# Kernel optimization log

Measured on AMD Instinct MI355X. Metric: run time of the kernel, lower is better.

Reference implementation:

```python
import jax, jax.numpy as jnp
import numpy as np

B, T, C, H = 2, 2048, 1024, 16
HD = C // H  # head dim = 64


def setup_inputs() -> dict:
    key = jax.random.key(0)
    k1, k2, k3 = jax.random.split(key, 3)
    scale = 0.02
    x = jax.random.normal(k1, (B, T, C), dtype=jnp.float32)
    w_attn = jax.random.normal(k2, (C, 3 * C), dtype=jnp.float32) * scale
    b_attn = jnp.zeros((3 * C,), dtype=jnp.float32)
    w_proj = jax.random.normal(k3, (C, C), dtype=jnp.float32) * scale
    b_proj = jnp.zeros((C,), dtype=jnp.float32)
    return {"x": x, "w_attn": w_attn, "b_attn": b_attn, "w_proj": w_proj, "b_proj": b_proj}


def reference(x, w_attn, b_attn, w_proj, b_proj):
    b, t, c = x.shape
    qkv = x @ w_attn + b_attn  # [B,T,3C]
    q, k, v = jnp.split(qkv, 3, axis=-1)
    # [B,T,C] -> [B,H,T,HD]
    q = q.reshape(b, t, H, HD).transpose(0, 2, 1, 3)
    k = k.reshape(b, t, H, HD).transpose(0, 2, 1, 3)
    v = v.reshape(b, t, H, HD).transpose(0, 2, 1, 3)
    att = jnp.einsum('bhqd,bhkd->bhqk', q, k) * (1.0 / jnp.sqrt(jnp.float32(HD)))
    causal = jnp.tril(jnp.ones((t, t), dtype=bool))  # [T,T]
    att = jnp.where(causal[None, None, :, :], att, jnp.float32(-jnp.inf))
    att = jax.nn.softmax(att, axis=-1)
    y = jnp.einsum('bhqk,bhkd->bhqd', att, v)
    y = y.transpose(0, 2, 1, 3).reshape(b, t, c)
    return y @ w_proj + b_proj
```

## Files before the change

### kernel.cpp

```cpp
#include <hip/hip_runtime.h>


typedef unsigned short u16;
typedef unsigned short u16x8 __attribute__((ext_vector_type(8)));
typedef __bf16 bf16x8 __attribute__((ext_vector_type(8)));
typedef __bf16 bf16x4 __attribute__((ext_vector_type(4)));
typedef float f32x4 __attribute__((ext_vector_type(4)));

#define MFMA16(a, b, c) __builtin_amdgcn_mfma_f32_16x16x32_bf16(a, b, c, 0, 0, 0)

static __device__ __forceinline__ u16 f2b(float f) {
  union { float f; unsigned int i; } x; x.f = f;
  unsigned int r = x.i + 0x7fffu + ((x.i >> 16) & 1u);
  return (u16)(r >> 16);
}
static __device__ __forceinline__ float b2f(u16 u) {
  union { unsigned int i; float f; } x; x.i = ((unsigned int)u) << 16; return x.f;
}

static __device__ __forceinline__ void gload_lds16(const u16* g, u16* l) {
#if defined(__HIP_DEVICE_COMPILE__)
  __builtin_amdgcn_global_load_lds(
      (const __attribute__((address_space(1))) unsigned int*)g,
      (__attribute__((address_space(3))) unsigned int*)l,
      16, 0, 0);
#else
  (void)g; (void)l;
#endif
}

__global__ __launch_bounds__(256) void cast_f32_bf16(
    const float* __restrict__ in, u16* __restrict__ out) {
  int i = (blockIdx.x * 256 + threadIdx.x) * 8;
  float4 a = *(const float4*)&in[i];
  float4 b = *(const float4*)&in[i + 4];
  u16x8 o;
  o[0] = f2b(a.x); o[1] = f2b(a.y); o[2] = f2b(a.z); o[3] = f2b(a.w);
  o[4] = f2b(b.x); o[5] = f2b(b.y); o[6] = f2b(b.z); o[7] = f2b(b.w);
  *(u16x8*)&out[i] = o;
}

__global__ __launch_bounds__(256) void transpose_f32_bf16(
    const float* __restrict__ in, u16* __restrict__ out, int R, int Cc) {
  __shared__ u16 tile[32][33];
  int bx = blockIdx.x, by = blockIdx.y;
  int tx = threadIdx.x, ty = threadIdx.y;
#pragma unroll
  for (int i = 0; i < 4; i++) {
    int r = by * 32 + ty + i * 8;
    int c = bx * 32 + tx;
    tile[ty + i * 8][tx] = f2b(in[r * Cc + c]);
  }
  __syncthreads();
#pragma unroll
  for (int i = 0; i < 4; i++) {
    int r = bx * 32 + ty + i * 8;
    int c = by * 32 + tx;
    out[r * R + c] = tile[tx][ty + i * 8];
  }
}

__global__ __launch_bounds__(256) void transpose_v(
    const u16* __restrict__ in, u16* __restrict__ out) {
  int bh = blockIdx.y;
  int t = blockIdx.x * 128 + (threadIdx.x & 127);
  int dg = (threadIdx.x >> 7) * 32;
  const u16* src = in + (bh * 2048 + t) * 64;
  int p = t & 31;
  int tp = (t & ~31) | ((((p >> 2) & 3) << 3) | ((p >> 4) << 2) | (p & 3));
  u16* dst = out + bh * 64 * 2048 + tp;
#pragma unroll
  for (int i = 0; i < 32; i++) {
    int d = dg + i;
    dst[d * 2048] = src[d];
  }
}

template <int MODE>
__global__ __launch_bounds__(256, 3) void gemm_bt(
    const u16* __restrict__ A, const u16* __restrict__ Bt,
    const float* __restrict__ bias, float* __restrict__ out,
    u16* __restrict__ Qb, u16* __restrict__ Kb, u16* __restrict__ Vb,
    int M, int N, int K) {
  __shared__ u16 lA[128 * 32];
  __shared__ u16 lB[128 * 32];

  const int tid = threadIdx.x;
  const int lane = tid & 63;
  const int w = tid >> 6;
  const int wm = (w >> 1) * 64, wn = (w & 1) * 64;
  const int l15 = lane & 15, quad = lane >> 4;
  const int m0 = blockIdx.y * 128, n0 = blockIdx.x * 128;

  const int srow = lane >> 2;
  const int scol = (lane & 3) * 8;

  f32x4 acc[4][4] = {};

  for (int k0 = 0; k0 < K; k0 += 32) {
    __syncthreads();
#pragma unroll
    for (int h = 0; h < 2; h++) {
      int r = h * 64 + w * 16 + srow;
      gload_lds16(&A[(m0 + r) * K + k0 + scol], &lA[h * 2048 + w * 512 + lane * 8]);
      gload_lds16(&Bt[(n0 + r) * K + k0 + scol], &lB[h * 2048 + w * 512 + lane * 8]);
    }
    __syncthreads();

    bf16x8 af[4], bfr[4];
#pragma unroll
    for (int mi = 0; mi < 4; mi++)
      af[mi] = *(const bf16x8*)&lA[(wm + mi * 16 + l15) * 32 + quad * 8];
#pragma unroll
    for (int ni = 0; ni < 4; ni++)
      bfr[ni] = *(const bf16x8*)&lB[(wn + ni * 16 + l15) * 32 + quad * 8];
#pragma unroll
    for (int mi = 0; mi < 4; mi++)
#pragma unroll
      for (int ni = 0; ni < 4; ni++)
        acc[mi][ni] = MFMA16(af[mi], bfr[ni], acc[mi][ni]);
  }

#pragma unroll
  for (int mi = 0; mi < 4; mi++) {
#pragma unroll
    for (int ni = 0; ni < 4; ni++) {
      int n = n0 + wn + ni * 16 + l15;
      float bv = bias[n];
#pragma unroll
      for (int reg = 0; reg < 4; reg++) {
        int m = m0 + wm + mi * 16 + quad * 4 + reg;
        float v = acc[mi][ni][reg] + bv;
        if (MODE == 1) {
          out[m * N + n] = v;
        } else {
          int which = n >> 10;
          if (which == 1) v *= 0.18033688011112042f;
          int hn = n & 1023;
          int hh = hn >> 6, d = hn & 63;
          int b = m >> 11, t = m & 2047;
          u16* dst = (which == 0) ? Qb : ((which == 1) ? Kb : Vb);
          dst[(((b << 4) + hh) * 2048 + t) * 64 + d] = f2b(v);
        }
      }
    }
  }
}

__global__ __launch_bounds__(256, 4) void attn_split(
    const u16* __restrict__ Qg, const u16* __restrict__ Kg,
    const u16* __restrict__ Vt, u16* __restrict__ Yg,
    u16* __restrict__ Opart, float* __restrict__ lpart) {
  __shared__ u16 lk[2][64 * 72];
  __shared__ u16 lvt[2][64 * 72];

  const int x = blockIdx.x;
  const int bh = blockIdx.y;
  int qt, s, ns;
  if (x < 8)       { qt = x;                s = 0;            ns = 1; }
  else if (x < 24) { int r = x - 8;  qt = 8  + (r >> 1); s = r & 1; ns = 2; }
  else if (x < 48) { int r = x - 24; qt = 16 + r / 3;    s = r % 3; ns = 3; }
  else             { int r = x - 48; qt = 24 + (r >> 2); s = r & 3; ns = 4; }
  const int total = qt + 1;
  const int kts  = (s * total) / ns;
  const int kend = ((s + 1) * total) / ns;

  const int tid = threadIdx.x;
  const int lane = tid & 63;
  const int w = tid >> 6;
  const int l15 = lane & 15, quad = lane >> 4;
  const int qbase = qt * 64;
  const int base = bh * 2048 * 64;
  const int vbase = bh * 64 * 2048;
  const int qloc = w * 16 + l15;

  const int sr = tid >> 3;
  const int sc = (tid & 7) * 8;

  const u16* qrow = Qg + base + (qbase + w * 16 + l15) * 64;
  bf16x8 bq0 = *(const bf16x8*)&qrow[quad * 8];
  bf16x8 bq1 = *(const bf16x8*)&qrow[32 + quad * 8];

  u16x8 onesu = {0x3F80, 0x3F80, 0x3F80, 0x3F80, 0x3F80, 0x3F80, 0x3F80, 0x3F80};
  bf16x8 ones = *(const bf16x8*)&onesu;

  const u16* kp = Kg + base;
  const u16* vp = Vt + vbase;

  u16x8 kr[2], vr[2];
  {
    int kvb = kts * 64;
#pragma unroll
    for (int h = 0; h < 2; h++) {
      int r = sr + h * 32;
      kr[h] = *(const u16x8*)&kp[(kvb + r) * 64 + sc];
      vr[h] = *(const u16x8*)&vp[r * 2048 + kvb + sc];
    }
  }

  f32x4 oacc[4] = {};
  f32x4 lacc = {};

  int cur = 0;
  for (int kt = kts; kt < kend; kt++) {
    u16* lkc = lk[cur];
    u16* lvc = lvt[cur];
#pragma unroll
    for (int h = 0; h < 2; h++) {
      int r = sr + h * 32;
      *(u16x8*)&lkc[r * 72 + sc] = kr[h];
      *(u16x8*)&lvc[r * 72 + sc] = vr[h];
    }
    __syncthreads();
    if (kt + 1 < kend) {
      int kvb = (kt + 1) * 64;
#pragma unroll
      for (int h = 0; h < 2; h++) {
        int r = sr + h * 32;
        kr[h] = *(const u16x8*)&kp[(kvb + r) * 64 + sc];
        vr[h] = *(const u16x8*)&vp[r * 2048 + kvb + sc];
      }
    }

    const bool diag = (kt == qt);

#pragma unroll
    for (int u = 0; u < 2; u++) {
      bf16x8 pa;
#pragma unroll
      for (int half = 0; half < 2; half++) {
        int nt = 2 * u + half;
        bf16x8 ak0 = *(const bf16x8*)&lkc[(nt * 16 + l15) * 72 + quad * 8];
        bf16x8 ak1 = *(const bf16x8*)&lkc[(nt * 16 + l15) * 72 + 32 + quad * 8];
        f32x4 st = {};
        st = MFMA16(ak0, bq0, st);
        st = MFMA16(ak1, bq1, st);
#pragma unroll
        for (int reg = 0; reg < 4; reg++) {
          float sv = st[reg];
          if (diag && (nt * 16 + quad * 4 + reg) > qloc) sv = -1e30f;
          pa[half * 4 + reg] = (__bf16)__builtin_amdgcn_exp2f(sv);
        }
      }
      lacc = MFMA16(pa, ones, lacc);
#pragma unroll
      for (int dt = 0; dt < 4; dt++) {
        bf16x8 bv = *(const bf16x8*)&lvc[(dt * 16 + l15) * 72 + u * 32 + quad * 8];
        oacc[dt] = MFMA16(pa, bv, oacc[dt]);
      }
    }
    cur ^= 1;
  }

  if (ns == 1) {
    const int b = bh >> 4, hh = bh & 15;
    float inv[4];
#pragma unroll
    for (int reg = 0; reg < 4; reg++) inv[reg] = 1.0f / lacc[reg];
#pragma unroll
    for (int dt = 0; dt < 4; dt++)
#pragma unroll
      for (int reg = 0; reg < 4; reg++) {
        int q = qbase + w * 16 + quad * 4 + reg;
        int col = hh * 64 + dt * 16 + l15;
        Yg[(b * 2048 + q) * 1024 + col] = f2b(oacc[dt][reg] * inv[reg]);
      }
  } else {
    const int p = bh * 80 + x;
    u16* op = Opart + p * 4096 + (w * 16) * 64;
#pragma unroll
    for (int dt = 0; dt < 4; dt++)
#pragma unroll
      for (int reg = 0; reg < 4; reg++)
        op[(quad * 4 + reg) * 64 + dt * 16 + l15] = f2b(oacc[dt][reg]);
    if (l15 == 0) {
#pragma unroll
      for (int reg = 0; reg < 4; reg++)
        lpart[p * 64 + w * 16 + quad * 4 + reg] = lacc[reg];
    }
  }
}

__global__ __launch_bounds__(256) void attn_combine(
    const u16* __restrict__ Opart, const float* __restrict__ lpart,
    u16* __restrict__ Yg) {
  const int qt = 8 + blockIdx.x;
  const int bh = blockIdx.y;
  const int tid = threadIdx.x;
  const int row = tid >> 2;
  const int cg = (tid & 3) * 16;
  int xb, ns;
  if (qt < 16)      { xb = 8  + (qt - 8) * 2;  ns = 2; }
  else if (qt < 24) { xb = 24 + (qt - 16) * 3; ns = 3; }
  else              { xb = 48 + (qt - 24) * 4; ns = 4; }

  float acc[16] = {};
  float lsum = 0.f;
  for (int i = 0; i < ns; i++) {
    int p = bh * 80 + xb + i;
    lsum += lpart[p * 64 + row];
    const u16* oprow = Opart + p * 4096 + row * 64 + cg;
    u16x8 a = *(const u16x8*)&oprow[0];
    u16x8 b = *(const u16x8*)&oprow[8];
#pragma unroll
    for (int j = 0; j < 8; j++) { acc[j] += b2f(a[j]); acc[8 + j] += b2f(b[j]); }
  }
  float inv = 1.0f / lsum;
  u16x8 o0, o1;
#pragma unroll
  for (int j = 0; j < 8; j++) { o0[j] = f2b(acc[j] * inv); o1[j] = f2b(acc[8 + j] * inv); }
  const int b = bh >> 4, hh = bh & 15;
  u16* y = Yg + ((long)(b * 2048 + qt * 64 + row)) * 1024 + hh * 64 + cg;
  *(u16x8*)&y[0] = o0;
  *(u16x8*)&y[8] = o1;
}

__global__ __launch_bounds__(256, 4) void attn_kernel(
    const u16* __restrict__ Qg, const u16* __restrict__ Kg,
    const u16* __restrict__ Vt, u16* __restrict__ Yg) {
  __shared__ u16 lk[64 * 72];
  __shared__ u16 lvt[64 * 72];

  const int qt = 31 - blockIdx.x;
  const int bh = blockIdx.y;
  const int tid = threadIdx.x;
  const int lane = tid & 63;
  const int w = tid >> 6;
  const int l15 = lane & 15, quad = lane >> 4;
  const int qbase = qt * 64;
  const int base = bh * 2048 * 64;
  const int vbase = bh * 64 * 2048;
  const int sr = tid >> 3;
  const int sc = (tid & 7) * 8;

  const u16* qrow = Qg + base + (qbase + w * 16 + l15) * 64;
  bf16x8 bq0 = *(const bf16x8*)&qrow[quad * 8];
  bf16x8 bq1 = *(const bf16x8*)&qrow[32 + quad * 8];

  u16x8 onesu = {0x3F80, 0x3F80, 0x3F80, 0x3F80, 0x3F80, 0x3F80, 0x3F80, 0x3F80};
  bf16x8 ones = *(const bf16x8*)&onesu;

  const u16* kp = Kg + base;
  const u16* vp = Vt + vbase;

  u16x8 kr[2], vr[2];
#pragma unroll
  for (int h = 0; h < 2; h++) {
    int r = sr + h * 32;
    kr[h] = *(const u16x8*)&kp[r * 64 + sc];
    vr[h] = *(const u16x8*)&vp[r * 2048 + sc];
  }

  f32x4 oacc[4] = {};
  f32x4 lacc = {};

  for (int kt = 0; kt <= qt; kt++) {
    __syncthreads();
#pragma unroll
    for (int h = 0; h < 2; h++) {
      int r = sr + h * 32;
      *(u16x8*)&lk[r * 72 + sc] = kr[h];
      *(u16x8*)&lvt[r * 72 + sc] = vr[h];
    }
    __syncthreads();
    if (kt < qt) {
      int kvb = (kt + 1) * 64;
#pragma unroll
      for (int h = 0; h < 2; h++) {
        int r = sr + h * 32;
        kr[h] = *(const u16x8*)&kp[(kvb + r) * 64 + sc];
        vr[h] = *(const u16x8*)&vp[r * 2048 + kvb + sc];
      }
    }

    const bool diag = (kt == qt);
    const int qloc = w * 16 + l15;
#pragma unroll
    for (int u = 0; u < 2; u++) {
      bf16x8 pa;
#pragma unroll
      for (int half = 0; half < 2; half++) {
        int nt = 2 * u + half;
        bf16x8 ak0 = *(const bf16x8*)&lk[(nt * 16 + l15) * 72 + quad * 8];
        bf16x8 ak1 = *(const bf16x8*)&lk[(nt * 16 + l15) * 72 + 32 + quad * 8];
        f32x4 st = {};
        st = MFMA16(ak0, bq0, st);
        st = MFMA16(ak1, bq1, st);
#pragma unroll
        for (int reg = 0; reg < 4; reg++) {
          float sv = st[reg];
          if (diag && (nt * 16 + quad * 4 + reg) > qloc) sv = -1e30f;
          pa[half * 4 + reg] = (__bf16)__builtin_amdgcn_exp2f(sv);
        }
      }
      lacc = MFMA16(pa, ones, lacc);
#pragma unroll
      for (int dt = 0; dt < 4; dt++) {
        bf16x8 bv = *(const bf16x8*)&lvt[(dt * 16 + l15) * 72 + u * 32 + quad * 8];
        oacc[dt] = MFMA16(pa, bv, oacc[dt]);
      }
    }
  }

  const int b = bh >> 4, hh = bh & 15;
  float inv[4];
#pragma unroll
  for (int reg = 0; reg < 4; reg++) inv[reg] = 1.0f / lacc[reg];
#pragma unroll
  for (int dt = 0; dt < 4; dt++)
#pragma unroll
    for (int reg = 0; reg < 4; reg++) {
      int q = qbase + w * 16 + quad * 4 + reg;
      int col = hh * 64 + dt * 16 + l15;
      Yg[(b * 2048 + q) * 1024 + col] = f2b(oacc[dt][reg] * inv[reg]);
    }
}

extern "C" void kernel_launch(void* const* d_in, const int* in_sizes, int n_in,
                              void* d_out, int out_size, void* d_ws, size_t ws_size,
                              hipStream_t stream) {
  const float* x      = (const float*)d_in[0];
  const float* w_attn = (const float*)d_in[1];
  const float* b_attn = (const float*)d_in[2];
  const float* w_proj = (const float*)d_in[3];
  const float* b_proj = (const float*)d_in[4];
  float* out = (float*)d_out;

  char* ws = (char*)d_ws;
  u16* wattnT = (u16*)(ws);
  u16* wprojT = (u16*)(ws + 6291456);
  u16* xb     = (u16*)(ws + 8388608);
  u16* Vt     = xb;
  u16* Qb     = (u16*)(ws + 16777216);
  u16* Kb     = (u16*)(ws + 25165824);
  u16* Vb     = (u16*)(ws + 33554432);
  u16* Yb     = (u16*)(ws + 41943040);
  u16* Opart  = (u16*)(ws + 50331648);
  float* lpart = (float*)(ws + 71303168);

  const bool split = (ws_size >= 71958528ULL);

  cast_f32_bf16<<<2048, 256, 0, stream>>>(x, xb);
  transpose_f32_bf16<<<dim3(96, 32), dim3(32, 8), 0, stream>>>(w_attn, wattnT, 1024, 3072);
  transpose_f32_bf16<<<dim3(32, 32), dim3(32, 8), 0, stream>>>(w_proj, wprojT, 1024, 1024);
  gemm_bt<0><<<dim3(24, 32), 256, 0, stream>>>(xb, wattnT, b_attn, nullptr,
                                               Qb, Kb, Vb, 4096, 3072, 1024);
  transpose_v<<<dim3(16, 32), 256, 0, stream>>>(Vb, Vt);
  if (split) {
    attn_split<<<dim3(80, 32), 256, 0, stream>>>(Qb, Kb, Vt, Yb, Opart, lpart);
    attn_combine<<<dim3(24, 32), 256, 0, stream>>>(Opart, lpart, Yb);
  } else {
    attn_kernel<<<dim3(32, 32), 256, 0, stream>>>(Qb, Kb, Vt, Yb);
  }
  gemm_bt<1><<<dim3(8, 32), 256, 0, stream>>>(Yb, wprojT, b_proj, out,
                                              nullptr, nullptr, nullptr, 4096, 1024, 1024);
}
```

Baseline: 195.1 us.

## Load K/V fragments directly from global memory, dropping LDS staging and barriers

Both attention kernels stop staging K and V^T tiles through shared memory with register prefetch and __syncthreads. Each wave now loads its MFMA operand fragments for every key tile straight from global memory into registers. This removes LDS traffic and barrier stalls. In exchange, the four waves of a block each fetch the same K/V data (a fourfold rise in global/L2 traffic), there is no explicit prefetch to hide load latency, and register pressure goes up.

```diff
diff --git a/kernel.cpp b/kernel.cpp
--- a/kernel.cpp
+++ b/kernel.cpp
@@ -151,9 +151,6 @@
     const u16* __restrict__ Qg, const u16* __restrict__ Kg,
     const u16* __restrict__ Vt, u16* __restrict__ Yg,
     u16* __restrict__ Opart, float* __restrict__ lpart) {
-  __shared__ u16 lk[2][64 * 72];
-  __shared__ u16 lvt[2][64 * 72];
-
   const int x = blockIdx.x;
   const int bh = blockIdx.y;
   int qt, s, ns;
@@ -174,9 +171,6 @@
   const int vbase = bh * 64 * 2048;
   const int qloc = w * 16 + l15;
 
-  const int sr = tid >> 3;
-  const int sc = (tid & 7) * 8;
-
   const u16* qrow = Qg + base + (qbase + w * 16 + l15) * 64;
   bf16x8 bq0 = *(const bf16x8*)&qrow[quad * 8];
   bf16x8 bq1 = *(const bf16x8*)&qrow[32 + quad * 8];
@@ -184,43 +178,27 @@
   u16x8 onesu = {0x3F80, 0x3F80, 0x3F80, 0x3F80, 0x3F80, 0x3F80, 0x3F80, 0x3F80};
   bf16x8 ones = *(const bf16x8*)&onesu;
 
-  const u16* kp = Kg + base;
-  const u16* vp = Vt + vbase;
-
-  u16x8 kr[2], vr[2];
-  {
-    int kvb = kts * 64;
-#pragma unroll
-    for (int h = 0; h < 2; h++) {
-      int r = sr + h * 32;
-      kr[h] = *(const u16x8*)&kp[(kvb + r) * 64 + sc];
-      vr[h] = *(const u16x8*)&vp[r * 2048 + kvb + sc];
-    }
-  }
+  const u16* kfp = Kg + base + l15 * 64 + quad * 8;
+  const u16* vfp = Vt + vbase + l15 * 2048 + quad * 8;
 
   f32x4 oacc[4] = {};
   f32x4 lacc = {};
 
-  int cur = 0;
   for (int kt = kts; kt < kend; kt++) {
-    u16* lkc = lk[cur];
-    u16* lvc = lvt[cur];
-#pragma unroll
-    for (int h = 0; h < 2; h++) {
-      int r = sr + h * 32;
-      *(u16x8*)&lkc[r * 72 + sc] = kr[h];
-      *(u16x8*)&lvc[r * 72 + sc] = vr[h];
-    }
-    __syncthreads();
-    if (kt + 1 < kend) {
-      int kvb = (kt + 1) * 64;
-#pragma unroll
-      for (int h = 0; h < 2; h++) {
-        int r = sr + h * 32;
-        kr[h] = *(const u16x8*)&kp[(kvb + r) * 64 + sc];
-        vr[h] = *(const u16x8*)&vp[r * 2048 + kvb + sc];
-      }
-    }
+    const int kvb = kt * 64;
+    bf16x8 ak[4][2];
+#pragma unroll
+    for (int nt = 0; nt < 4; nt++) {
+      const u16* p = kfp + (kvb + nt * 16) * 64;
+      ak[nt][0] = *(const bf16x8*)&p[0];
+      ak[nt][1] = *(const bf16x8*)&p[32];
+    }
+    bf16x8 bv[2][4];
+#pragma unroll
+    for (int u = 0; u < 2; u++)
+#pragma unroll
+      for (int dt = 0; dt < 4; dt++)
+        bv[u][dt] = *(const bf16x8*)&vfp[dt * 16 * 2048 + kvb + u * 32];
 
     const bool diag = (kt == qt);
 
@@ -230,11 +208,9 @@
 #pragma unroll
       for (int half = 0; half < 2; half++) {
         int nt = 2 * u + half;
-        bf16x8 ak0 = *(const bf16x8*)&lkc[(nt * 16 + l15) * 72 + quad * 8];
-        bf16x8 ak1 = *(const bf16x8*)&lkc[(nt * 16 + l15) * 72 + 32 + quad * 8];
         f32x4 st = {};
-        st = MFMA16(ak0, bq0, st);
-        st = MFMA16(ak1, bq1, st);
+        st = MFMA16(ak[nt][0], bq0, st);
+        st = MFMA16(ak[nt][1], bq1, st);
 #pragma unroll
         for (int reg = 0; reg < 4; reg++) {
           float sv = st[reg];
@@ -244,12 +220,9 @@
       }
       lacc = MFMA16(pa, ones, lacc);
 #pragma unroll
-      for (int dt = 0; dt < 4; dt++) {
-        bf16x8 bv = *(const bf16x8*)&lvc[(dt * 16 + l15) * 72 + u * 32 + quad * 8];
-        oacc[dt] = MFMA16(pa, bv, oacc[dt]);
-      }
-    }
-    cur ^= 1;
+      for (int dt = 0; dt < 4; dt++)
+        oacc[dt] = MFMA16(pa, bv[u][dt], oacc[dt]);
+    }
   }
 
   if (ns == 1) {
@@ -318,9 +291,6 @@
 __global__ __launch_bounds__(256, 4) void attn_kernel(
     const u16* __restrict__ Qg, const u16* __restrict__ Kg,
     const u16* __restrict__ Vt, u16* __restrict__ Yg) {
-  __shared__ u16 lk[64 * 72];
-  __shared__ u16 lvt[64 * 72];
-
   const int qt = 31 - blockIdx.x;
   const int bh = blockIdx.y;
   const int tid = threadIdx.x;
@@ -330,8 +300,7 @@
   const int qbase = qt * 64;
   const int base = bh * 2048 * 64;
   const int vbase = bh * 64 * 2048;
-  const int sr = tid >> 3;
-  const int sc = (tid & 7) * 8;
+  const int qloc = w * 16 + l15;
 
   const u16* qrow = Qg + base + (qbase + w * 16 + l15) * 64;
   bf16x8 bq0 = *(const bf16x8*)&qrow[quad * 8];
@@ -340,52 +309,38 @@
   u16x8 onesu = {0x3F80, 0x3F80, 0x3F80, 0x3F80, 0x3F80, 0x3F80, 0x3F80, 0x3F80};
   bf16x8 ones = *(const bf16x8*)&onesu;
 
-  const u16* kp = Kg + base;
-  const u16* vp = Vt + vbase;
-
-  u16x8 kr[2], vr[2];
-#pragma unroll
-  for (int h = 0; h < 2; h++) {
-    int r = sr + h * 32;
-    kr[h] = *(const u16x8*)&kp[r * 64 + sc];
-    vr[h] = *(const u16x8*)&vp[r * 2048 + sc];
-  }
+  const u16* kfp = Kg + base + l15 * 64 + quad * 8;
+  const u16* vfp = Vt + vbase + l15 * 2048 + quad * 8;
 
   f32x4 oacc[4] = {};
   f32x4 lacc = {};
 
   for (int kt = 0; kt <= qt; kt++) {
-    __syncthreads();
-#pragma unroll
-    for (int h = 0; h < 2; h++) {
-      int r = sr + h * 32;
-      *(u16x8*)&lk[r * 72 + sc] = kr[h];
-      *(u16x8*)&lvt[r * 72 + sc] = vr[h];
-    }
-    __syncthreads();
-    if (kt < qt) {
-      int kvb = (kt + 1) * 64;
-#pragma unroll
-      for (int h = 0; h < 2; h++) {
-        int r = sr + h * 32;
-        kr[h] = *(const u16x8*)&kp[(kvb + r) * 64 + sc];
-        vr[h] = *(const u16x8*)&vp[r * 2048 + kvb + sc];
-      }
-    }
+    const int kvb = kt * 64;
+    bf16x8 ak[4][2];
+#pragma unroll
+    for (int nt = 0; nt < 4; nt++) {
+      const u16* p = kfp + (kvb + nt * 16) * 64;
+      ak[nt][0] = *(const bf16x8*)&p[0];
+      ak[nt][1] = *(const bf16x8*)&p[32];
+    }
+    bf16x8 bv[2][4];
+#pragma unroll
+    for (int u = 0; u < 2; u++)
+#pragma unroll
+      for (int dt = 0; dt < 4; dt++)
+        bv[u][dt] = *(const bf16x8*)&vfp[dt * 16 * 2048 + kvb + u * 32];
 
     const bool diag = (kt == qt);
-    const int qloc = w * 16 + l15;
 #pragma unroll
     for (int u = 0; u < 2; u++) {
       bf16x8 pa;
 #pragma unroll
       for (int half = 0; half < 2; half++) {
         int nt = 2 * u + half;
-        bf16x8 ak0 = *(const bf16x8*)&lk[(nt * 16 + l15) * 72 + quad * 8];
-        bf16x8 ak1 = *(const bf16x8*)&lk[(nt * 16 + l15) * 72 + 32 + quad * 8];
         f32x4 st = {};
-        st = MFMA16(ak0, bq0, st);
-        st = MFMA16(ak1, bq1, st);
+        st = MFMA16(ak[nt][0], bq0, st);
+        st = MFMA16(ak[nt][1], bq1, st);
 #pragma unroll
         for (int reg = 0; reg < 4; reg++) {
           float sv = st[reg];
@@ -395,10 +350,8 @@
       }
       lacc = MFMA16(pa, ones, lacc);
 #pragma unroll
-      for (int dt = 0; dt < 4; dt++) {
-        bf16x8 bv = *(const bf16x8*)&lvt[(dt * 16 + l15) * 72 + u * 32 + quad * 8];
-        oacc[dt] = MFMA16(pa, bv, oacc[dt]);
-      }
+      for (int dt = 0; dt < 4; dt++)
+        oacc[dt] = MFMA16(pa, bv[u][dt], oacc[dt]);
     }
   }
 
```

Measured after the change: 309.9 us. +58.8%, slower.
